# Kernel optimization log

Measured on AMD Instinct MI355X. Metric: run time of the kernel, lower is better.

Reference implementation:

```python
import jax, jax.numpy as jnp
import numpy as np

B, SEQ, H = 256, 200, 256
NFFT, HOP = 16, 8
FREQ = NFFT // 2 + 1          # 9
NSEG = SEQ // HOP + 1         # 26 (SEQ % HOP == 0 -> pad_len == 0)
FACTOR = 2


def _gelu(x):
    return jax.nn.gelu(x, approximate=False)  # torch nn.GELU / F.gelu default = exact erf


def _layernorm(x, w, b, eps=1e-12):
    u = x.mean(-1, keepdims=True)
    s = ((x - u) ** 2).mean(-1, keepdims=True)
    return w * (x - u) / jnp.sqrt(s + eps) + b


def _mixer(xr, xi, w1, b1, w2, b2):
    # complex MLP: einsum '...ijk,jkl->...ijl' with per-kept-dim weights
    e = lambda a, w: jnp.einsum('bijk,jkl->bijl', a, w)
    o1r = _gelu(e(xr, w1[0]) - e(xi, w1[1]) + b1[0])
    o1i = _gelu(e(xi, w1[0]) + e(xr, w1[1]) + b1[1])
    o2r = e(o1r, w2[0]) - e(o1i, w2[1]) + b2[0]
    # NOTE: faithful to the source bug: o1_image used in BOTH terms of o2_image
    o2i = e(o1i, w2[0]) + e(o1i, w2[1]) + b2[1]
    return o2r, o2i


def _stft(x):
    # torch.stft(n_fft=NFFT, hop=HOP, center=True, onesided=True, normalized=True,
    #            pad_mode='constant', window=None -> rectangular ones)
    pad = NFFT // 2
    xp = jnp.pad(x, ((0, 0), (pad, pad)))
    idx = jnp.arange(NSEG)[:, None] * HOP + jnp.arange(NFFT)[None, :]
    frames = xp[:, idx]                                    # [N, NSEG, NFFT]
    spec = jnp.fft.rfft(frames, axis=-1) * (NFFT ** -0.5)  # normalized=True
    return jnp.swapaxes(spec, -1, -2)                      # [N, FREQ, NSEG]


def _istft(spec):
    # torch.istft(center=True, normalized=True, rectangular window)
    n = spec.shape[0]
    frames = jnp.fft.irfft(jnp.swapaxes(spec, -1, -2) * (NFFT ** 0.5), n=NFFT, axis=-1)
    L = (NSEG - 1) * HOP + NFFT
    idx = (jnp.arange(NSEG)[:, None] * HOP + jnp.arange(NFFT)[None, :]).ravel()
    y = jnp.zeros((n, L), frames.dtype).at[:, idx].add(frames.reshape(n, -1))
    env = jnp.zeros((L,), frames.dtype).at[idx].add(1.0)   # window**2 overlap-add
    pad = NFFT // 2
    out_len = (NSEG - 1) * HOP                              # = SEQ
    return y[:, pad:pad + out_len] / env[pad:pad + out_len]


def setup_inputs() -> dict:
    key = jax.random.key(0)
    ks = jax.random.split(key, 24)
    p = lambda k, sh: jax.random.normal(k, sh, jnp.float32) * 0.02
    d = {}
    d["input_tensor"] = jax.random.normal(ks[0], (B, SEQ, H), jnp.float32)
    # grouped conv2d: weight [NSEG, 1, H, FREQ] -> stored as [NSEG, H, FREQ]
    d["conv_w"] = p(ks[1], (NSEG, H, FREQ)); d["conv_b"] = p(ks[2], (NSEG,))
    d["fm_w1"] = p(ks[3], (2, NSEG, FREQ, FREQ * FACTOR)); d["fm_b1"] = p(ks[4], (2, NSEG, FREQ * FACTOR))
    d["fm_w2"] = p(ks[5], (2, NSEG, FREQ * FACTOR, FREQ)); d["fm_b2"] = p(ks[6], (2, NSEG, FREQ))
    d["cm_w1"] = p(ks[7], (2, NSEG, H, H * FACTOR)); d["cm_b1"] = p(ks[8], (2, NSEG, H * FACTOR))
    d["cm_w2"] = p(ks[9], (2, NSEG, H * FACTOR, H)); d["cm_b2"] = p(ks[10], (2, NSEG, H))
    d["sm_w1"] = p(ks[11], (2, FREQ, NSEG, NSEG * FACTOR)); d["sm_b1"] = p(ks[12], (2, FREQ, NSEG * FACTOR))
    d["sm_w2"] = p(ks[13], (2, FREQ, NSEG * FACTOR, NSEG)); d["sm_b2"] = p(ks[14], (2, FREQ, NSEG))
    d["ln_w"] = jnp.ones((H,), jnp.float32); d["ln_b"] = jnp.zeros((H,), jnp.float32)
    d["ff_w1"] = p(ks[15], (H, 4 * H)); d["ff_b1"] = p(ks[16], (4 * H,))
    d["ff_w2"] = p(ks[17], (4 * H, H)); d["ff_b2"] = p(ks[18], (H,))
    d["ff_ln_w"] = jnp.ones((H,), jnp.float32); d["ff_ln_b"] = jnp.zeros((H,), jnp.float32)
    return d


def reference(input_tensor, conv_w, conv_b, fm_w1, fm_b1, fm_w2, fm_b2,
              cm_w1, cm_b1, cm_w2, cm_b2, sm_w1, sm_b1, sm_w2, sm_b2,
              ln_w, ln_b, ff_w1, ff_b1, ff_w2, ff_b2, ff_ln_w, ff_ln_b):
    b, seq, h = input_tensor.shape
    x = jnp.swapaxes(input_tensor, -1, -2).reshape(b * h, seq)  # pad_len == 0
    spec = _stft(x).reshape(b, h, FREQ, NSEG)
    xr, xi = spec.real, spec.imag
    xnorm = jnp.sqrt(xr ** 2 + xi ** 2)                         # [b,h,F,S]
    # grouped conv2d with full (H,FREQ) kernel == per-segment weighted sum
    w = jnp.einsum('bhfs,shf->bs', xnorm, conv_w) + conv_b
    w = w + jnp.exp(jnp.arange(1 - NSEG, 1, dtype=jnp.float32))  # exp decay bias
    xr = xr * w[:, None, None, :]
    xi = xi * w[:, None, None, :]
    # -> [b,h,S,F]: frequency mixing (kept=segment, mixed=freq)
    xr = jnp.swapaxes(xr, -1, -2); xi = jnp.swapaxes(xi, -1, -2)
    xr, xi = _mixer(xr, xi, fm_w1, fm_b1, fm_w2, fm_b2)
    # -> [b,F,S,h]: channel mixing (kept=segment, mixed=hidden)
    xr = jnp.swapaxes(xr, 1, 3); xi = jnp.swapaxes(xi, 1, 3)
    xr, xi = _mixer(xr, xi, cm_w1, cm_b1, cm_w2, cm_b2)
    # -> [b,h,F,S]: segment mixing (kept=freq, mixed=segment)
    xr = jnp.transpose(xr, (0, 3, 1, 2)); xi = jnp.transpose(xi, (0, 3, 1, 2))
    xr, xi = _mixer(xr, xi, sm_w1, sm_b1, sm_w2, sm_b2)
    spec = (xr + 1j * xi).reshape(b * h, FREQ, NSEG)
    y = _istft(spec)[:, :seq].reshape(b, h, seq)
    y = jnp.swapaxes(y, -1, -2)                                  # [b,seq,h]
    hs = _layernorm(y + input_tensor, ln_w, ln_b)                # dropout p=0
    ff = _gelu(hs @ ff_w1 + ff_b1) @ ff_w2 + ff_b2
    return _layernorm(ff + hs, ff_ln_w, ff_ln_b)
```

## Files before the change

### kernel.cpp

```cpp
#include <hip/hip_runtime.h>
#include <hip/hip_bf16.h>
#include <math.h>

typedef __hip_bfloat16 bf16;
typedef short bf16x8 __attribute__((ext_vector_type(8)));
typedef float f32x4 __attribute__((ext_vector_type(4)));

#define B_    256
#define SEQ_  200
#define H_    256
#define FREQ_ 9
#define NSEG_ 26
#define LDS64 64

__device__ __forceinline__ float ldb(const bf16* p, size_t i){ return __bfloat162float(p[i]); }
__device__ __forceinline__ void stb(bf16* p, size_t i, float v){ p[i] = __float2bfloat16(v); }
__device__ __forceinline__ short f2b(float v){ union{bf16 b; short s;} c; c.b = __float2bfloat16(v); return c.s; }
__device__ __forceinline__ unsigned short f2bu(float v){ union{bf16 b; unsigned short s;} c; c.b = __float2bfloat16(v); return c.s; }
__device__ __forceinline__ float gelu_(float x){
  float y  = 0.7978845608f*(x + 0.044715f*x*x*x);
  float ay = fabsf(y);
  float e  = __expf(-2.f*ay);
  float th = 1.f - 2.f*e*__builtin_amdgcn_rcpf(1.f + e);
  th = copysignf(th, y);
  return 0.5f*x*(1.f + th);
}

__device__ __constant__ float CT16[16] = {
  1.0f, 0.9238795325f, 0.7071067812f, 0.3826834324f, 0.0f, -0.3826834324f, -0.7071067812f, -0.9238795325f,
 -1.0f,-0.9238795325f,-0.7071067812f,-0.3826834324f, 0.0f,  0.3826834324f, 0.7071067812f,  0.9238795325f};
__device__ __constant__ float ST16[16] = {
  0.0f, 0.3826834324f, 0.7071067812f, 0.9238795325f, 1.0f,  0.9238795325f, 0.7071067812f,  0.3826834324f,
  0.0f,-0.3826834324f,-0.7071067812f,-0.9238795325f,-1.0f, -0.9238795325f,-0.7071067812f, -0.3826834324f};

__device__ __forceinline__ void gload16(const short* g, short* l){
  __builtin_amdgcn_global_load_lds(
      (const __attribute__((address_space(1))) unsigned int*)(const void*)g,
      (__attribute__((address_space(3))) unsigned int*)(void*)l, 16, 0, 0);
}

template<int ROWS>
__device__ __forceinline__ void stage_tile(short* lds, const short* src, int rstride, int tid){
  int rl = tid >> 3;
  int c  = tid & 7;
  #pragma unroll
  for(int p=0; p<ROWS/32; p++){
    int r = p*32 + rl;
    int csrc = c ^ (r & 7);
    gload16(src + (size_t)r*rstride + csrc*8, lds + r*LDS64 + c*8);
  }
}

__device__ __forceinline__ void mma_bk64(const short* lA, const short* lB, int wm, int wn,
                                         int lane, f32x4 acc[4][4]){
  int m_l = lane & 15, quad = lane >> 4;
  int sw = m_l & 7;
  #pragma unroll
  for(int ks=0; ks<64; ks+=32){
    int cs = (((ks>>3) + quad) ^ sw) * 8;
    bf16x8 a[4], b[4];
    #pragma unroll
    for(int i=0;i<4;i++) a[i] = *(const bf16x8*)&lA[(wm + i*16 + m_l)*LDS64 + cs];
    #pragma unroll
    for(int j=0;j<4;j++) b[j] = *(const bf16x8*)&lB[(wn + j*16 + m_l)*LDS64 + cs];
    #pragma unroll
    for(int i=0;i<4;i++)
      #pragma unroll
      for(int j=0;j<4;j++)
        acc[i][j] = __builtin_amdgcn_mfma_f32_16x16x32_bf16(a[i], b[j], acc[i][j], 0,0,0);
  }
}

__global__ __launch_bounds__(256) void k_prep_b1(const float* __restrict__ w1, short* __restrict__ B1t){
  int g = blockIdx.x;
  int jt = g & 7, ht = (g>>3)&3, p = (g>>5)&1, s = g>>6;
  __shared__ float tile[64][65];
  int t = threadIdx.x;
  const float* src = w1 + (size_t)p*3407872 + (size_t)s*131072;
  #pragma unroll
  for(int q=0;q<16;q++){
    int r = q*4 + (t>>6), c = t & 63;
    tile[r][c] = src[(size_t)(ht*64 + r)*512 + jt*64 + c];
  }
  __syncthreads();
  int n_l = t >> 2, kc = (t & 3)*16;
  short tA[16] __attribute__((aligned(16)));
  short tB[16] __attribute__((aligned(16)));
  #pragma unroll
  for(int i=0;i<16;i++){
    float v = tile[kc+i][n_l];
    tA[i] = (p==0) ? f2b(v) : f2b(-v);
    tB[i] = f2b(v);
  }
  int j = jt*64 + n_l, h = ht*64 + kc;
  size_t d1, d2;
  if(p==0){ d1 = ((size_t)(s*1024 + j))*512 + h;
            d2 = ((size_t)(s*1024 + 512 + j))*512 + 256 + h; }
  else    { d1 = ((size_t)(s*1024 + j))*512 + 256 + h;
            d2 = ((size_t)(s*1024 + 512 + j))*512 + h; }
  *(int4*)&B1t[d1] = *(int4*)&tA[0]; *(int4*)&B1t[d1+8] = *(int4*)&tA[8];
  *(int4*)&B1t[d2] = *(int4*)&tB[0]; *(int4*)&B1t[d2+8] = *(int4*)&tB[8];
}

__global__ __launch_bounds__(256) void k_prep_b2(const float* __restrict__ w2,
                                                 short* __restrict__ B2r, short* __restrict__ B2i){
  int g = blockIdx.x;
  int ht = g & 3, jt = (g>>2)&7, s = g>>5;
  __shared__ float t0[64][65], t1[64][65];
  int t = threadIdx.x;
  const float* s0 = w2 + (size_t)s*131072;
  const float* s1 = w2 + 3407872 + (size_t)s*131072;
  #pragma unroll
  for(int q=0;q<16;q++){
    int r = q*4 + (t>>6), c = t & 63;
    t0[r][c] = s0[(size_t)(jt*64 + r)*256 + ht*64 + c];
    t1[r][c] = s1[(size_t)(jt*64 + r)*256 + ht*64 + c];
  }
  __syncthreads();
  int n_l = t >> 2, jc = (t & 3)*16;
  short ta[16] __attribute__((aligned(16)));
  short tb[16] __attribute__((aligned(16)));
  short tc[16] __attribute__((aligned(16)));
  #pragma unroll
  for(int i=0;i<16;i++){
    float v0 = t0[jc+i][n_l], v1 = t1[jc+i][n_l];
    ta[i] = f2b(v0); tb[i] = f2b(-v1); tc[i] = f2b(v0+v1);
  }
  int n = ht*64 + n_l, j = jt*64 + jc;
  size_t dr = ((size_t)(s*256 + n))*1024 + j;
  size_t di = ((size_t)(s*256 + n))*512 + j;
  *(int4*)&B2r[dr]     = *(int4*)&ta[0]; *(int4*)&B2r[dr+8]     = *(int4*)&ta[8];
  *(int4*)&B2r[dr+512] = *(int4*)&tb[0]; *(int4*)&B2r[dr+520]   = *(int4*)&tb[8];
  *(int4*)&B2i[di]     = *(int4*)&tc[0]; *(int4*)&B2i[di+8]     = *(int4*)&tc[8];
}

__global__ __launch_bounds__(256) void k_transp(const float* __restrict__ src, short* __restrict__ dst,
                                                int R, int C){
  int ct = blockIdx.x % (C/64);
  int rt = blockIdx.x / (C/64);
  __shared__ float tile[64][65];
  int t = threadIdx.x;
  #pragma unroll
  for(int p=0;p<16;p++){
    int r = p*4 + (t>>6), c = t & 63;
    tile[r][c] = src[(size_t)(rt*64 + r)*C + ct*64 + c];
  }
  __syncthreads();
  int row_out = t >> 2, rc = (t & 3)*16;
  short tmp[16] __attribute__((aligned(16)));
  #pragma unroll
  for(int i=0;i<16;i++) tmp[i] = f2b(tile[rc+i][row_out]);
  size_t base = (size_t)(ct*64 + row_out)*R + rt*64 + rc;
  *(int4*)&dst[base] = *(int4*)&tmp[0]; *(int4*)&dst[base+8] = *(int4*)&tmp[8];
}

__global__ __launch_bounds__(256) void k_prep_sm(const float* __restrict__ w1, const float* __restrict__ w2,
                                                 short* __restrict__ B1sm, short* __restrict__ B2sm){
  int f = blockIdx.x;
  int t = threadIdx.x;
  for(int idx=t; idx<8192; idx+=256){
    int jp = idx >> 6, k = idx & 63;
    float v = 0.f;
    if(jp < 104){
      int j = (jp < 52) ? jp : jp - 52;
      if(k < 26){
        int s = k;
        v = (jp < 52) ? w1[f*1352 + s*52 + j] : w1[12168 + f*1352 + s*52 + j];
      } else if(k >= 32 && k < 58){
        int s = k - 32;
        v = (jp < 52) ? -w1[12168 + f*1352 + s*52 + j] : w1[f*1352 + s*52 + j];
      }
    }
    B1sm[(size_t)f*8192 + idx] = f2b(v);
  }
  for(int idx=t; idx<8192; idx+=256){
    int sop = idx >> 7, k = idx & 127;
    float v = 0.f;
    if(sop < 26){
      if(k < 52)       v = w2[f*1352 + k*26 + sop];
      else if(k < 104) v = -w2[12168 + f*1352 + (k-52)*26 + sop];
    } else if(sop < 52){
      int so = sop - 26;
      if(k >= 52 && k < 104)
        v = w2[f*1352 + (k-52)*26 + so] + w2[12168 + f*1352 + (k-52)*26 + so];
    }
    B2sm[(size_t)f*8192 + idx] = f2b(v);
  }
}

__global__ __launch_bounds__(256) void k_prep_fm(const float* __restrict__ w1, const float* __restrict__ w2,
                                                 short* __restrict__ B1fm, short* __restrict__ B2fm){
  int s = blockIdx.x;
  int t = threadIdx.x;
  for(int idx=t; idx<1536; idx+=256){
    int n = idx >> 5, k = idx & 31;
    float v = 0.f;
    if(n < 18){
      if(k < 9)       v = w1[s*162 + k*18 + n];
      else if(k < 18) v = -w1[4212 + s*162 + (k-9)*18 + n];
    } else if(n < 36){
      int j = n - 18;
      if(k < 9)       v = w1[4212 + s*162 + k*18 + j];
      else if(k < 18) v = w1[s*162 + (k-9)*18 + j];
    }
    B1fm[s*1536 + idx] = f2b(v);
  }
  for(int idx=t; idx<2048; idx+=256){
    int n = idx >> 6, k = idx & 63;
    float v = 0.f;
    if(n < 9){
      if(k < 18)      v = w2[s*162 + k*9 + n];
      else if(k < 36) v = -w2[4212 + s*162 + (k-18)*9 + n];
    } else if(n < 18){
      int f = n - 9;
      if(k >= 18 && k < 36)
        v = w2[s*162 + (k-18)*9 + f] + w2[4212 + s*162 + (k-18)*9 + f];
    }
    B2fm[s*2048 + idx] = f2b(v);
  }
}

#define LX1 40
#define LG1 72
__global__ __launch_bounds__(256) void k_sfm2(const float* __restrict__ inp,
                                              const float* __restrict__ cw, const float* __restrict__ cb,
                                              const short* __restrict__ B1fm, const short* __restrict__ B2fm,
                                              const float* __restrict__ bb1, const float* __restrict__ bb2,
                                              bf16* __restrict__ oR, bf16* __restrict__ oI){
  int blk = blockIdx.x; int b = blk / NSEG_; int s = blk % NSEG_; int t = threadIdx.x;
  int lane = t & 63, wave = t >> 6, m_l = lane & 15, quad = lane >> 4;
  __shared__ __align__(16) short sm[20736];
  __shared__ float red[256];
  __shared__ float lb1f[48];
  short* lX  = sm;
  short* lB1 = sm + 10240;
  short* lG  = sm;
  short* lB2 = sm + 18432;

  {
    const short* src1 = B1fm + s*1536;
    for(int idx=t; idx<768; idx+=256){
      int r = idx >> 4, c = idx & 15;
      *(unsigned*)&lB1[r*LX1 + c*2] = *(const unsigned*)&src1[r*32 + c*2];
    }
    const short* src2 = B2fm + s*2048;
    for(int idx=t; idx<1024; idx+=256){
      int r = idx >> 5, c = idx & 31;
      *(unsigned*)&lB2[r*LG1 + c*2] = *(const unsigned*)&src2[r*64 + c*2];
    }
    if(t < 48) lb1f[t] = (t < 18) ? bb1[s*18 + t] : (t < 36 ? bb1[468 + s*18 + (t-18)] : 0.f);
  }

  float xv[16];
  int t0 = s*8 - 8;
  #pragma unroll
  for(int k=0;k<16;k++){
    int tt = t0 + k;
    xv[k] = (tt>=0 && tt<SEQ_) ? inp[(size_t)(b*SEQ_+tt)*H_ + t] : 0.0f;
  }
  float xr[9], xi[9];
  float acc = 0.f;
  #pragma unroll
  for(int f=0;f<FREQ_;f++){
    float ar=0.f, ai=0.f;
    #pragma unroll
    for(int k=0;k<16;k++){
      int m = (f*k) & 15;
      ar += xv[k]*CT16[m];
      ai -= xv[k]*ST16[m];
    }
    xr[f] = 0.25f*ar; xi[f] = 0.25f*ai;
    acc += sqrtf(xr[f]*xr[f] + xi[f]*xi[f]) * cw[(s*H_+t)*FREQ_ + f];
  }

  red[t] = acc; __syncthreads();
  for(int off=128; off>0; off>>=1){ if(t<off) red[t] += red[t+off]; __syncthreads(); }
  float wv = red[0] + cb[s] + __expf((float)(s - (NSEG_-1)));

  {
    float vb[32];
    #pragma unroll
    for(int f=0;f<9;f++){ vb[f] = xr[f]*wv; vb[9+f] = xi[f]*wv; }
    #pragma unroll
    for(int k=18;k<32;k++) vb[k] = 0.f;
    #pragma unroll
    for(int c=0;c<16;c++){
      unsigned u = (unsigned)f2bu(vb[2*c]) | ((unsigned)f2bu(vb[2*c+1]) << 16);
      *(unsigned*)&lX[t*LX1 + c*2] = u;
    }
  }
  __syncthreads();

  int h0 = wave*64;
  f32x4 acc1[4][3];
  #pragma unroll
  for(int i=0;i<4;i++)
    #pragma unroll
    for(int j=0;j<3;j++) acc1[i][j] = (f32x4){0.f,0.f,0.f,0.f};
  {
    bf16x8 a1[4], b1v[3];
    #pragma unroll
    for(int i=0;i<4;i++) a1[i] = *(const bf16x8*)&lX[(h0 + i*16 + m_l)*LX1 + quad*8];
    #pragma unroll
    for(int j=0;j<3;j++) b1v[j] = *(const bf16x8*)&lB1[(j*16 + m_l)*LX1 + quad*8];
    #pragma unroll
    for(int i=0;i<4;i++)
      #pragma unroll
      for(int j=0;j<3;j++)
        acc1[i][j] = __builtin_amdgcn_mfma_f32_16x16x32_bf16(a1[i], b1v[j], acc1[i][j], 0,0,0);
  }
  __syncthreads();

  #pragma unroll
  for(int i=0;i<4;i++){
    #pragma unroll
    for(int j=0;j<3;j++){
      int n = j*16 + m_l;
      float bias = lb1f[n];
      #pragma unroll
      for(int r=0;r<4;r++){
        int row = h0 + i*16 + quad*4 + r;
        lG[row*LG1 + n] = f2b(gelu_(acc1[i][j][r] + bias));
      }
    }
  }
  #pragma unroll
  for(int c=0;c<8;c++) *(unsigned*)&lG[t*LG1 + 48 + c*2] = 0u;
  __syncthreads();

  f32x4 acc2[4][2];
  #pragma unroll
  for(int i=0;i<4;i++)
    #pragma unroll
    for(int j=0;j<2;j++) acc2[i][j] = (f32x4){0.f,0.f,0.f,0.f};
  #pragma unroll
  for(int ks=0; ks<64; ks+=32){
    bf16x8 a2[4], b2v[2];
    #pragma unroll
    for(int i=0;i<4;i++) a2[i] = *(const bf16x8*)&lG[(h0 + i*16 + m_l)*LG1 + ks + quad*8];
    #pragma unroll
    for(int j=0;j<2;j++) b2v[j] = *(const bf16x8*)&lB2[(j*16 + m_l)*LG1 + ks + quad*8];
    #pragma unroll
    for(int i=0;i<4;i++)
      #pragma unroll
      for(int j=0;j<2;j++)
        acc2[i][j] = __builtin_amdgcn_mfma_f32_16x16x32_bf16(a2[i], b2v[j], acc2[i][j], 0,0,0);
  }

  #pragma unroll
  for(int j=0;j<2;j++){
    int n = j*16 + m_l;
    if(n < 18){
      bool isI = n >= 9;
      int f = isI ? n-9 : n;
      float bias = isI ? bb2[234 + s*9 + f] : bb2[s*9 + f];
      bf16* outp = isI ? oI : oR;
      size_t base = ((size_t)(s*B_ + b)*FREQ_ + f)*H_;
      #pragma unroll
      for(int i=0;i<4;i++){
        int h = h0 + i*16 + quad*4;
        short pk[4] __attribute__((aligned(8)));
        #pragma unroll
        for(int r=0;r<4;r++) pk[r] = f2b(acc2[i][j][r] + bias);
        *(int2*)&outp[base + h] = *(const int2*)&pk[0];
      }
    }
  }
}

__global__ __launch_bounds__(256) void k_cm1(const bf16* __restrict__ Xr, const bf16* __restrict__ Xi,
                                             const short* __restrict__ B1t, const float* __restrict__ b1bias,
                                             short* __restrict__ H, int half){
  int nt = blockIdx.x & 7, mt = (blockIdx.x >> 3) % 9, s = blockIdx.x / 72;
  int tid = threadIdx.x, lane = tid & 63, wave = tid >> 6;
  int wm = (wave & 1)*64, wn = (wave >> 1)*64;
  __shared__ __align__(16) short lA[128*LDS64];
  __shared__ __align__(16) short lB[128*LDS64];
  f32x4 acc[4][4];
  #pragma unroll
  for(int i=0;i<4;i++)
    #pragma unroll
    for(int j=0;j<4;j++) acc[i][j] = (f32x4){0.f,0.f,0.f,0.f};
  int rowbase = half*1152 + mt*128;
  const short* Bbase = B1t + ((size_t)(s*1024 + nt*128))*512;
  for(int k0=0; k0<512; k0+=64){
    const short* Asrc = (k0 < 256)
      ? (const short*)(Xr + ((size_t)(s*2304 + rowbase))*256 + k0)
      : (const short*)(Xi + ((size_t)(s*2304 + rowbase))*256 + (k0-256));
    stage_tile<128>(lA, Asrc, 256, tid);
    stage_tile<128>(lB, Bbase + k0, 512, tid);
    __syncthreads();
    mma_bk64(lA, lB, wm, wn, lane, acc);
    __syncthreads();
  }
  int m_l = lane & 15, quad = lane >> 4;
  #pragma unroll
  for(int i=0;i<4;i++){
    #pragma unroll
    for(int j=0;j<4;j++){
      int n = nt*128 + wn + j*16 + m_l;
      float bias = (n < 512) ? b1bias[s*512 + n] : b1bias[13312 + s*512 + (n-512)];
      #pragma unroll
      for(int r=0;r<4;r++){
        int mrow = wm + i*16 + quad*4 + r;
        float v = gelu_(acc[i][j][r] + bias);
        H[((size_t)(s*1152 + mt*128 + mrow))*1024 + n] = f2b(v);
      }
    }
  }
}

__global__ __launch_bounds__(256) void k_cm2(const short* __restrict__ H,
                                             const short* __restrict__ B2r, const short* __restrict__ B2i,
                                             const float* __restrict__ b2bias,
                                             bf16* __restrict__ oR, bf16* __restrict__ oI, int half){
  int nt = blockIdx.x & 3, mt = (blockIdx.x>>2) % 9, s = blockIdx.x / 36;
  int tid = threadIdx.x, lane = tid & 63, wave = tid >> 6;
  int wm = (wave & 1)*64, wn = (wave >> 1)*64;
  bool isOi = nt >= 2;
  int n0 = (nt & 1)*128;
  int K = isOi ? 512 : 1024;
  int Aoff = isOi ? 512 : 0;
  int Bstride = isOi ? 512 : 1024;
  const short* Bb = isOi ? (B2i + ((size_t)(s*256 + n0))*512) : (B2r + ((size_t)(s*256 + n0))*1024);
  const short* Ab = H + ((size_t)(s*1152 + mt*128))*1024 + Aoff;
  __shared__ __align__(16) short lA[128*LDS64];
  __shared__ __align__(16) short lB[128*LDS64];
  f32x4 acc[4][4];
  #pragma unroll
  for(int i=0;i<4;i++)
    #pragma unroll
    for(int j=0;j<4;j++) acc[i][j] = (f32x4){0.f,0.f,0.f,0.f};
  for(int k0=0; k0<K; k0+=64){
    stage_tile<128>(lA, Ab + k0, 1024, tid);
    stage_tile<128>(lB, Bb + k0, Bstride, tid);
    __syncthreads();
    mma_bk64(lA, lB, wm, wn, lane, acc);
    __syncthreads();
  }
  int m_l = lane & 15, quad = lane >> 4;
  bf16* outp = isOi ? oI : oR;
  #pragma unroll
  for(int i=0;i<4;i++){
    #pragma unroll
    for(int j=0;j<4;j++){
      int n = n0 + wn + j*16 + m_l;
      float bias = b2bias[(isOi ? 6656 : 0) + s*256 + n];
      #pragma unroll
      for(int r=0;r<4;r++){
        int mrow = wm + i*16 + quad*4 + r;
        int rowg = half*1152 + mt*128 + mrow;
        stb(outp, ((size_t)rowg*NSEG_ + s)*256 + n, acc[i][j][r] + bias);
      }
    }
  }
}

#define LDX 72
#define LDG 136
__global__ __launch_bounds__(256) void k_smm(const bf16* __restrict__ iR, const bf16* __restrict__ iI,
                                             const short* __restrict__ B1sm, const short* __restrict__ B2sm,
                                             const float* __restrict__ bb1, const float* __restrict__ bb2,
                                             bf16* __restrict__ oR, bf16* __restrict__ oI){
  int blk = blockIdx.x;
  int f  = blk % 9;
  int hh = (blk/9) & 1;
  int bq = blk / 18;
  int t = threadIdx.x, lane = t & 63, wave = t >> 6;
  int m_l = lane & 15, quad = lane >> 4;
  __shared__ __align__(16) short sm[18432 + 8704];
  __shared__ float lb1[128];
  short* lX  = sm;
  short* lB1 = sm + 128*LDX;
  short* lG  = sm;
  short* lB2 = sm + 18432;
  int rbase = (bq*9 + f)*26;

  #pragma unroll
  for(int it=0; it<4; it++){
    int idx = it*256 + t;
    int r = idx >> 3, c = idx & 7;
    *(int4*)&lB1[r*LDX + c*8] = *(const int4*)&B1sm[(size_t)f*8192 + r*64 + c*8];
  }
  #pragma unroll
  for(int it=0; it<4; it++){
    int idx = it*256 + t;
    int r = idx >> 4, c = idx & 15;
    *(int4*)&lB2[r*LDG + c*8] = *(const int4*)&B2sm[(size_t)f*8192 + r*128 + c*8];
  }
  if(t < 128) lb1[t] = (t < 52) ? bb1[f*52 + t] : (t < 104 ? bb1[468 + f*52 + (t-52)] : 0.f);

  int hl = t & 127, g = t >> 7;
  #pragma unroll
  for(int it=0; it<13; it++){
    int a   = it*2 + g;
    int arr = a >= 13;
    int pr  = arr ? a-13 : a;
    int s0  = pr*2;
    const bf16* src = arr ? iI : iR;
    unsigned v0 = *(const unsigned short*)&src[((size_t)(rbase+s0  ))*256 + hh*128 + hl];
    unsigned v1 = *(const unsigned short*)&src[((size_t)(rbase+s0+1))*256 + hh*128 + hl];
    *(unsigned*)&lX[hl*LDX + arr*32 + s0] = v0 | (v1 << 16);
  }
  {
    int zb = g ? 58 : 26;
    #pragma unroll
    for(int i=0;i<3;i++) *(unsigned*)&lX[hl*LDX + zb + i*2] = 0u;
  }
  __syncthreads();

  int h0 = wave*32;
  f32x4 acc1[2][8];
  #pragma unroll
  for(int i=0;i<2;i++)
    #pragma unroll
    for(int j=0;j<8;j++) acc1[i][j] = (f32x4){0.f,0.f,0.f,0.f};
  #pragma unroll
  for(int ks=0; ks<64; ks+=32){
    bf16x8 av[2], bv[8];
    #pragma unroll
    for(int i=0;i<2;i++) av[i] = *(const bf16x8*)&lX[(h0 + i*16 + m_l)*LDX + ks + quad*8];
    #pragma unroll
    for(int j=0;j<8;j++) bv[j] = *(const bf16x8*)&lB1[(j*16 + m_l)*LDX + ks + quad*8];
    #pragma unroll
    for(int i=0;i<2;i++)
      #pragma unroll
      for(int j=0;j<8;j++)
        acc1[i][j] = __builtin_amdgcn_mfma_f32_16x16x32_bf16(av[i], bv[j], acc1[i][j], 0,0,0);
  }
  __syncthreads();

  #pragma unroll
  for(int i=0;i<2;i++){
    #pragma unroll
    for(int j=0;j<8;j++){
      int jp = j*16 + m_l;
      float bias = lb1[jp];
      #pragma unroll
      for(int r=0;r<4;r++){
        int hrow = h0 + i*16 + quad*4 + r;
        lG[hrow*LDG + jp] = f2b(gelu_(acc1[i][j][r] + bias));
      }
    }
  }
  __syncthreads();

  f32x4 acc2[2][4];
  #pragma unroll
  for(int i=0;i<2;i++)
    #pragma unroll
    for(int j=0;j<4;j++) acc2[i][j] = (f32x4){0.f,0.f,0.f,0.f};
  #pragma unroll
  for(int ks=0; ks<128; ks+=32){
    bf16x8 av[2], bv[4];
    #pragma unroll
    for(int i=0;i<2;i++) av[i] = *(const bf16x8*)&lG[(h0 + i*16 + m_l)*LDG + ks + quad*8];
    #pragma unroll
    for(int j=0;j<4;j++) bv[j] = *(const bf16x8*)&lB2[(j*16 + m_l)*LDG + ks + quad*8];
    #pragma unroll
    for(int i=0;i<2;i++)
      #pragma unroll
      for(int j=0;j<4;j++)
        acc2[i][j] = __builtin_amdgcn_mfma_f32_16x16x32_bf16(av[i], bv[j], acc2[i][j], 0,0,0);
  }

  #pragma unroll
  for(int j=0;j<4;j++){
    int sop = j*16 + m_l;
    if(sop < 52){
      int arr = sop >= 26;
      int so  = sop - (arr ? 26 : 0);
      float bias = bb2[(arr ? 234 : 0) + f*26 + so];
      bf16* outp = arr ? oI : oR;
      #pragma unroll
      for(int i=0;i<2;i++){
        int h = hh*128 + h0 + i*16 + quad*4;
        short pk[4] __attribute__((aligned(8)));
        #pragma unroll
        for(int r=0;r<4;r++) pk[r] = f2b(acc2[i][j][r] + bias);
        *(int2*)&outp[((size_t)(rbase + so))*256 + h] = *(const int2*)&pk[0];
      }
    }
  }
}

__global__ __launch_bounds__(256) void k_ist(const bf16* __restrict__ iR, const bf16* __restrict__ iI,
                                             const float* __restrict__ inp,
                                             const float* __restrict__ lnw, const float* __restrict__ lnb,
                                             float* __restrict__ hs, bf16* __restrict__ hsb){
  int blk = blockIdx.x; int b = blk / SEQ_; int t = blk % SEQ_; int h = threadIdx.x;
  int l = t + 8;
  int s2 = l >> 3, k2 = l & 7;
  int s1 = s2 - 1, k1 = k2 + 8;
  float acc = 0.f;
  #pragma unroll
  for(int p=0;p<2;p++){
    int s = p ? s2 : s1;
    int k = p ? k2 : k1;
    size_t base = (size_t)(b*FREQ_)*NSEG_;
    float v = ldb(iR, (base + 0*NSEG_ + s)*256 + h);
    float a8 = ldb(iR, (base + 8*NSEG_ + s)*256 + h);
    v += (k & 1) ? -a8 : a8;
    #pragma unroll
    for(int f=1;f<8;f++){
      int m = (f*k) & 15;
      float rr = ldb(iR, (base + f*NSEG_ + s)*256 + h);
      float ii = ldb(iI, (base + f*NSEG_ + s)*256 + h);
      v += 2.f*(rr*CT16[m] - ii*ST16[m]);
    }
    acc += 0.25f*v;
  }
  float z = 0.5f*acc + inp[(size_t)(b*SEQ_+t)*H_ + h];

  __shared__ float red[256];
  red[h] = z; __syncthreads();
  for(int off=128; off>0; off>>=1){ if(h<off) red[h] += red[h+off]; __syncthreads(); }
  float u = red[0] * (1.f/256.f);
  __syncthreads();
  float d = z - u;
  red[h] = d*d; __syncthreads();
  for(int off=128; off>0; off>>=1){ if(h<off) red[h] += red[h+off]; __syncthreads(); }
  float var = red[0] * (1.f/256.f);
  float o = lnw[h]*d*rsqrtf(var + 1e-12f) + lnb[h];
  size_t oi = (size_t)(b*SEQ_+t)*H_ + h;
  hs[oi] = o;
  stb(hsb, oi, o);
}

__global__ __launch_bounds__(256) void k_ff1m(const short* __restrict__ hsb, const short* __restrict__ fw1t,
                                              const float* __restrict__ fb1, short* __restrict__ hid, int row0){
  int nt = blockIdx.x & 7, mt = blockIdx.x >> 3;
  int tid = threadIdx.x, lane = tid & 63, wave = tid >> 6;
  int wm = (wave & 1)*64, wn = (wave >> 1)*64;
  __shared__ __align__(16) short lA[128*LDS64];
  __shared__ __align__(16) short lB[128*LDS64];
  f32x4 acc[4][4];
  #pragma unroll
  for(int i=0;i<4;i++)
    #pragma unroll
    for(int j=0;j<4;j++) acc[i][j] = (f32x4){0.f,0.f,0.f,0.f};
  const short* Ab = hsb + ((size_t)(row0 + mt*128))*256;
  const short* Bb = fw1t + ((size_t)(nt*128))*256;
  for(int k0=0; k0<256; k0+=64){
    stage_tile<128>(lA, Ab + k0, 256, tid);
    stage_tile<128>(lB, Bb + k0, 256, tid);
    __syncthreads();
    mma_bk64(lA, lB, wm, wn, lane, acc);
    __syncthreads();
  }
  int m_l = lane & 15, quad = lane >> 4;
  #pragma unroll
  for(int i=0;i<4;i++){
    #pragma unroll
    for(int j=0;j<4;j++){
      int n = nt*128 + wn + j*16 + m_l;
      float bias = fb1[n];
      #pragma unroll
      for(int r=0;r<4;r++){
        int mrow = wm + i*16 + quad*4 + r;
        hid[((size_t)(mt*128 + mrow))*1024 + n] = f2b(gelu_(acc[i][j][r] + bias));
      }
    }
  }
}

__global__ __launch_bounds__(256) void k_ff2m(const short* __restrict__ hid, const short* __restrict__ fw2t,
                                              const float* __restrict__ fb2, const float* __restrict__ hs,
                                              const float* __restrict__ lnw, const float* __restrict__ lnb,
                                              float* __restrict__ out, int row0){
  int mt = blockIdx.x;
  int tid = threadIdx.x, lane = tid & 63, wave = tid >> 6;
  int wn = wave*64;
  __shared__ __align__(16) short lA[64*LDS64];
  __shared__ __align__(16) short lB[256*LDS64];
  __shared__ float ssum[64][4], ssq[64][4];
  f32x4 acc[4][4];
  #pragma unroll
  for(int i=0;i<4;i++)
    #pragma unroll
    for(int j=0;j<4;j++) acc[i][j] = (f32x4){0.f,0.f,0.f,0.f};
  const short* Ab = hid + ((size_t)(mt*64))*1024;
  for(int k0=0; k0<1024; k0+=64){
    stage_tile<64>(lA, Ab + k0, 1024, tid);
    stage_tile<256>(lB, fw2t + k0, 1024, tid);
    __syncthreads();
    mma_bk64(lA, lB, 0, wn, lane, acc);
    __syncthreads();
  }
  int m_l = lane & 15, quad = lane >> 4;
  int rowg0 = row0 + mt*64;
  #pragma unroll
  for(int i=0;i<4;i++){
    #pragma unroll
    for(int j=0;j<4;j++){
      int col = wn + j*16 + m_l;
      float bias = fb2[col];
      #pragma unroll
      for(int r=0;r<4;r++){
        int mrow = i*16 + quad*4 + r;
        acc[i][j][r] += bias + hs[(size_t)(rowg0+mrow)*256 + col];
      }
    }
  }
  #pragma unroll
  for(int i=0;i<4;i++){
    #pragma unroll
    for(int r=0;r<4;r++){
      float sv = 0.f, sq = 0.f;
      #pragma unroll
      for(int j=0;j<4;j++){ float v = acc[i][j][r]; sv += v; sq += v*v; }
      #pragma unroll
      for(int msk=1; msk<16; msk<<=1){ sv += __shfl_xor(sv, msk); sq += __shfl_xor(sq, msk); }
      if(m_l == 0){ int mrow = i*16 + quad*4 + r; ssum[mrow][wave] = sv; ssq[mrow][wave] = sq; }
    }
  }
  __syncthreads();
  if(tid < 64){
    float s1 = ssum[tid][0]+ssum[tid][1]+ssum[tid][2]+ssum[tid][3];
    float s2 = ssq[tid][0]+ssq[tid][1]+ssq[tid][2]+ssq[tid][3];
    float mean = s1*(1.f/256.f);
    float var  = s2*(1.f/256.f) - mean*mean;
    ssum[tid][0] = mean;
    ssq[tid][0]  = rsqrtf(var + 1e-12f);
  }
  __syncthreads();
  #pragma unroll
  for(int i=0;i<4;i++){
    #pragma unroll
    for(int j=0;j<4;j++){
      int col = wn + j*16 + m_l;
      float gw = lnw[col], gb = lnb[col];
      #pragma unroll
      for(int r=0;r<4;r++){
        int mrow = i*16 + quad*4 + r;
        float mean = ssum[mrow][0], inv = ssq[mrow][0];
        out[(size_t)(rowg0+mrow)*256 + col] = (acc[i][j][r] - mean)*inv*gw + gb;
      }
    }
  }
}

extern "C" void kernel_launch(void* const* d_in, const int* in_sizes, int n_in,
                              void* d_out, int out_size, void* d_ws, size_t ws_size,
                              hipStream_t stream){
  const float* inp    = (const float*)d_in[0];
  const float* conv_w = (const float*)d_in[1];
  const float* conv_b = (const float*)d_in[2];
  const float* fm_w1  = (const float*)d_in[3];
  const float* fm_b1  = (const float*)d_in[4];
  const float* fm_w2  = (const float*)d_in[5];
  const float* fm_b2  = (const float*)d_in[6];
  const float* cm_w1  = (const float*)d_in[7];
  const float* cm_b1  = (const float*)d_in[8];
  const float* cm_w2  = (const float*)d_in[9];
  const float* cm_b2  = (const float*)d_in[10];
  const float* sm_w1  = (const float*)d_in[11];
  const float* sm_b1  = (const float*)d_in[12];
  const float* sm_w2  = (const float*)d_in[13];
  const float* sm_b2  = (const float*)d_in[14];
  const float* ln_w   = (const float*)d_in[15];
  const float* ln_b   = (const float*)d_in[16];
  const float* ff_w1  = (const float*)d_in[17];
  const float* ff_b1  = (const float*)d_in[18];
  const float* ff_w2  = (const float*)d_in[19];
  const float* ff_b2  = (const float*)d_in[20];
  const float* ffln_w = (const float*)d_in[21];
  const float* ffln_b = (const float*)d_in[22];
  float* out = (float*)d_out;

  const size_t NS = (size_t)B_ * NSEG_ * FREQ_ * H_;
  const size_t HN = (size_t)NSEG_ * 1152 * 1024;
  short* ws = (short*)d_ws;
  bf16*  b0   = (bf16*)ws;
  bf16*  b1   = (bf16*)(ws + NS);
  bf16*  b2   = (bf16*)(ws + 2*NS);
  bf16*  b3   = (bf16*)(ws + 3*NS);
  short* H    = ws + 4*NS;
  short* B1t  = H + HN;
  short* B2r  = B1t + (size_t)26*1024*512;
  short* B2i  = B2r + (size_t)26*256*1024;
  short* fw1t = B2i + (size_t)26*256*512;
  short* fw2t = fw1t + 262144;
  short* B1sm = fw2t + 262144;
  short* B2sm = B1sm + 73728;
  short* B1fm = B2sm + 73728;
  short* B2fm = B1fm + 39936;
  float* hs   = (float*)b0;
  bf16*  hsb  = (bf16*)H;
  short* hid  = (short*)b2;

  k_prep_b1<<<1664, 256, 0, stream>>>(cm_w1, B1t);
  k_prep_b2<<<832,  256, 0, stream>>>(cm_w2, B2r, B2i);
  k_transp <<<64,   256, 0, stream>>>(ff_w1, fw1t, 256, 1024);
  k_transp <<<64,   256, 0, stream>>>(ff_w2, fw2t, 1024, 256);
  k_prep_sm<<<9,    256, 0, stream>>>(sm_w1, sm_w2, B1sm, B2sm);
  k_prep_fm<<<26,   256, 0, stream>>>(fm_w1, fm_w2, B1fm, B2fm);

  k_sfm2<<<B_*NSEG_, 256, 0, stream>>>(inp, conv_w, conv_b, B1fm, B2fm, fm_b1, fm_b2, b2, b3);
  for(int half=0; half<2; half++){
    k_cm1<<<26*72, 256, 0, stream>>>(b2, b3, B1t, cm_b1, H, half);
    k_cm2<<<26*36, 256, 0, stream>>>(H, B2r, B2i, cm_b2, b0, b1, half);
  }
  k_smm<<<B_*2*FREQ_, 256, 0, stream>>>(b0, b1, B1sm, B2sm, sm_b1, sm_b2, b2, b3);
  k_ist<<<B_*SEQ_,  256, 0, stream>>>(b2, b3, inp, ln_w, ln_b, hs, hsb);
  for(int c=0; c<2; c++){
    int row0 = c*25600;
    k_ff1m<<<1600, 256, 0, stream>>>((const short*)hsb, fw1t, ff_b1, hid, row0);
    k_ff2m<<<400,  256, 0, stream>>>(hid, fw2t, ff_b2, hs, ffln_w, ffln_b, out, row0);
  }
}
```

Before: 893.3 us.

## Batch iSTFT+LayerNorm over 8 timesteps per block and pretranspose conv weights

The iSTFT/LayerNorm kernel now has each block handle 8 consecutive timesteps that share the same two segments. The spectrum is loaded once per block instead of once per timestep, and the two LDS tree reductions are replaced with wave shuffles that compute sum and sum of squares in a single pass. Separately, conv weights are pretransposed so the STFT kernel reads them coalesced, and its LDS stores are packed into 16-byte writes. The single-pass variance (E[x²]−mean²) is less numerically stable than the previous two-pass form.

```diff
diff --git a/kernel.cpp b/kernel.cpp
--- a/kernel.cpp
+++ b/kernel.cpp
@@ -220,10 +220,19 @@
   }
 }
 
+__global__ __launch_bounds__(256) void k_prep_cw(const float* __restrict__ cw, float* __restrict__ cwT){
+  int s = blockIdx.x; int t = threadIdx.x;
+  __shared__ float tile[2304];
+  for(int i=t; i<2304; i+=256) tile[i] = cw[s*2304 + i];
+  __syncthreads();
+  #pragma unroll
+  for(int f=0; f<9; f++) cwT[(s*9+f)*256 + t] = tile[t*9+f];
+}
+
 #define LX1 40
 #define LG1 72
 __global__ __launch_bounds__(256) void k_sfm2(const float* __restrict__ inp,
-                                              const float* __restrict__ cw, const float* __restrict__ cb,
+                                              const float* __restrict__ cwT, const float* __restrict__ cb,
                                               const short* __restrict__ B1fm, const short* __restrict__ B2fm,
                                               const float* __restrict__ bb1, const float* __restrict__ bb2,
                                               bf16* __restrict__ oR, bf16* __restrict__ oI){
@@ -251,6 +260,10 @@
     if(t < 48) lb1f[t] = (t < 18) ? bb1[s*18 + t] : (t < 36 ? bb1[468 + s*18 + (t-18)] : 0.f);
   }
 
+  float cwv[9];
+  #pragma unroll
+  for(int f=0;f<9;f++) cwv[f] = cwT[(s*9+f)*256 + t];
+
   float xv[16];
   int t0 = s*8 - 8;
   #pragma unroll
@@ -270,7 +283,7 @@
       ai -= xv[k]*ST16[m];
     }
     xr[f] = 0.25f*ar; xi[f] = 0.25f*ai;
-    acc += sqrtf(xr[f]*xr[f] + xi[f]*xi[f]) * cw[(s*H_+t)*FREQ_ + f];
+    acc += sqrtf(xr[f]*xr[f] + xi[f]*xi[f]) * cwv[f];
   }
 
   red[t] = acc; __syncthreads();
@@ -283,11 +296,12 @@
     for(int f=0;f<9;f++){ vb[f] = xr[f]*wv; vb[9+f] = xi[f]*wv; }
     #pragma unroll
     for(int k=18;k<32;k++) vb[k] = 0.f;
-    #pragma unroll
-    for(int c=0;c<16;c++){
-      unsigned u = (unsigned)f2bu(vb[2*c]) | ((unsigned)f2bu(vb[2*c+1]) << 16);
-      *(unsigned*)&lX[t*LX1 + c*2] = u;
-    }
+    union { unsigned u[16]; int4 v4[4]; } pk;
+    #pragma unroll
+    for(int c=0;c<16;c++)
+      pk.u[c] = (unsigned)f2bu(vb[2*c]) | ((unsigned)f2bu(vb[2*c+1]) << 16);
+    #pragma unroll
+    for(int q=0;q<4;q++) *(int4*)&lX[t*LX1 + q*8] = pk.v4[q];
   }
   __syncthreads();
 
@@ -584,47 +598,61 @@
   }
 }
 
-__global__ __launch_bounds__(256) void k_ist(const bf16* __restrict__ iR, const bf16* __restrict__ iI,
-                                             const float* __restrict__ inp,
-                                             const float* __restrict__ lnw, const float* __restrict__ lnb,
-                                             float* __restrict__ hs, bf16* __restrict__ hsb){
-  int blk = blockIdx.x; int b = blk / SEQ_; int t = blk % SEQ_; int h = threadIdx.x;
-  int l = t + 8;
-  int s2 = l >> 3, k2 = l & 7;
-  int s1 = s2 - 1, k1 = k2 + 8;
-  float acc = 0.f;
+__global__ __launch_bounds__(256) void k_ist8(const bf16* __restrict__ iR, const bf16* __restrict__ iI,
+                                              const float* __restrict__ inp,
+                                              const float* __restrict__ lnw, const float* __restrict__ lnb,
+                                              float* __restrict__ hs, bf16* __restrict__ hsb){
+  int blk = blockIdx.x; int b = blk / 25; int o = blk % 25; int h = threadIdx.x;
+  int lane = h & 63, wave = h >> 6;
+  float rr[2][9], ii[2][8];
   #pragma unroll
   for(int p=0;p<2;p++){
-    int s = p ? s2 : s1;
-    int k = p ? k2 : k1;
-    size_t base = (size_t)(b*FREQ_)*NSEG_;
-    float v = ldb(iR, (base + 0*NSEG_ + s)*256 + h);
-    float a8 = ldb(iR, (base + 8*NSEG_ + s)*256 + h);
-    v += (k & 1) ? -a8 : a8;
+    int s = o + p;
+    size_t base = (size_t)b*FREQ_*NSEG_ + s;
+    #pragma unroll
+    for(int f=0;f<9;f++) rr[p][f] = ldb(iR, (base + f*NSEG_)*256 + h);
+    #pragma unroll
+    for(int f=1;f<8;f++) ii[p][f] = ldb(iI, (base + f*NSEG_)*256 + h);
+  }
+  float z[8];
+  #pragma unroll
+  for(int dt=0; dt<8; dt++){
+    float v  = rr[0][0] + rr[1][0];
+    float s8 = rr[0][8] + rr[1][8];
+    v += (dt & 1) ? -s8 : s8;
     #pragma unroll
     for(int f=1;f<8;f++){
-      int m = (f*k) & 15;
-      float rr = ldb(iR, (base + f*NSEG_ + s)*256 + h);
-      float ii = ldb(iI, (base + f*NSEG_ + s)*256 + h);
-      v += 2.f*(rr*CT16[m] - ii*ST16[m]);
-    }
-    acc += 0.25f*v;
-  }
-  float z = 0.5f*acc + inp[(size_t)(b*SEQ_+t)*H_ + h];
-
-  __shared__ float red[256];
-  red[h] = z; __syncthreads();
-  for(int off=128; off>0; off>>=1){ if(h<off) red[h] += red[h+off]; __syncthreads(); }
-  float u = red[0] * (1.f/256.f);
-  __syncthreads();
-  float d = z - u;
-  red[h] = d*d; __syncthreads();
-  for(int off=128; off>0; off>>=1){ if(h<off) red[h] += red[h+off]; __syncthreads(); }
-  float var = red[0] * (1.f/256.f);
-  float o = lnw[h]*d*rsqrtf(var + 1e-12f) + lnb[h];
-  size_t oi = (size_t)(b*SEQ_+t)*H_ + h;
-  hs[oi] = o;
-  stb(hsb, oi, o);
+      int m1 = (f*(dt+8)) & 15;
+      int m2 = (f*dt) & 15;
+      v += 2.f*(rr[0][f]*CT16[m1] - ii[0][f]*ST16[m1]);
+      v += 2.f*(rr[1][f]*CT16[m2] - ii[1][f]*ST16[m2]);
+    }
+    int t = o*8 + dt;
+    z[dt] = 0.125f*v + inp[(size_t)(b*SEQ_+t)*H_ + h];
+  }
+  __shared__ float wsum[8][4], wsq[8][4];
+  #pragma unroll
+  for(int dt=0; dt<8; dt++){
+    float sv = z[dt], sq = z[dt]*z[dt];
+    #pragma unroll
+    for(int msk=1; msk<64; msk<<=1){ sv += __shfl_xor(sv, msk); sq += __shfl_xor(sq, msk); }
+    if(lane == 0){ wsum[dt][wave] = sv; wsq[dt][wave] = sq; }
+  }
+  __syncthreads();
+  float gw = lnw[h], gb = lnb[h];
+  #pragma unroll
+  for(int dt=0; dt<8; dt++){
+    float s1 = wsum[dt][0]+wsum[dt][1]+wsum[dt][2]+wsum[dt][3];
+    float s2 = wsq[dt][0]+wsq[dt][1]+wsq[dt][2]+wsq[dt][3];
+    float mean = s1*(1.f/256.f);
+    float var  = s2*(1.f/256.f) - mean*mean;
+    float inv  = rsqrtf(var + 1e-12f);
+    float ov = gw*(z[dt]-mean)*inv + gb;
+    int t = o*8 + dt;
+    size_t oi = (size_t)(b*SEQ_+t)*H_ + h;
+    hs[oi] = ov;
+    stb(hsb, oi, ov);
+  }
 }
 
 __global__ __launch_bounds__(256) void k_ff1m(const short* __restrict__ hsb, const short* __restrict__ fw1t,
@@ -785,6 +813,7 @@
   short* B2sm = B1sm + 73728;
   short* B1fm = B2sm + 73728;
   short* B2fm = B1fm + 39936;
+  float* cwT  = (float*)(B2fm + 53248);
   float* hs   = (float*)b0;
   bf16*  hsb  = (bf16*)H;
   short* hid  = (short*)b2;
@@ -795,14 +824,15 @@
   k_transp <<<64,   256, 0, stream>>>(ff_w2, fw2t, 1024, 256);
   k_prep_sm<<<9,    256, 0, stream>>>(sm_w1, sm_w2, B1sm, B2sm);
   k_prep_fm<<<26,   256, 0, stream>>>(fm_w1, fm_w2, B1fm, B2fm);
-
-  k_sfm2<<<B_*NSEG_, 256, 0, stream>>>(inp, conv_w, conv_b, B1fm, B2fm, fm_b1, fm_b2, b2, b3);
+  k_prep_cw<<<26,   256, 0, stream>>>(conv_w, cwT);
+
+  k_sfm2<<<B_*NSEG_, 256, 0, stream>>>(inp, cwT, conv_b, B1fm, B2fm, fm_b1, fm_b2, b2, b3);
   for(int half=0; half<2; half++){
     k_cm1<<<26*72, 256, 0, stream>>>(b2, b3, B1t, cm_b1, H, half);
     k_cm2<<<26*36, 256, 0, stream>>>(H, B2r, B2i, cm_b2, b0, b1, half);
   }
   k_smm<<<B_*2*FREQ_, 256, 0, stream>>>(b0, b1, B1sm, B2sm, sm_b1, sm_b2, b2, b3);
-  k_ist<<<B_*SEQ_,  256, 0, stream>>>(b2, b3, inp, ln_w, ln_b, hs, hsb);
+  k_ist8<<<B_*25, 256, 0, stream>>>(b2, b3, inp, ln_w, ln_b, hs, hsb);
   for(int c=0; c<2; c++){
     int row0 = c*25600;
     k_ff1m<<<1600, 256, 0, stream>>>((const short*)hsb, fw1t, ff_b1, hid, row0);
```

After: 840.3 us. -5.9%, faster.
